# Optimization experiments

Hardware: AMD Instinct MI355X
Metric: run time of the kernel (lower is better)

Reference implementation:

```python
import jax, jax.numpy as jnp
import numpy as np

EMBED = 1024
HEADS = 16
HEAD_DIM = EMBED // HEADS
B, S = 4, 2048


def setup_inputs() -> dict:
    key = jax.random.key(0)
    ks = jax.random.split(key, 13)
    scale = 1.0 / np.sqrt(EMBED)
    inp = {
        "query": jax.random.normal(ks[0], (B, S, EMBED), dtype=jnp.float32),
        "key": jax.random.normal(ks[1], (B, S, EMBED), dtype=jnp.float32),
        "value": jax.random.normal(ks[2], (B, S, EMBED), dtype=jnp.float32),
        "mask": jax.random.randint(ks[3], (B, 1, S, S), 0, 2) > 0,
        "Wq": jax.random.normal(ks[4], (EMBED, EMBED), dtype=jnp.float32) * scale,
        "bq": jnp.zeros((EMBED,), dtype=jnp.float32),
        "Wk": jax.random.normal(ks[5], (EMBED, EMBED), dtype=jnp.float32) * scale,
        "bk": jnp.zeros((EMBED,), dtype=jnp.float32),
        "Wv": jax.random.normal(ks[6], (EMBED, EMBED), dtype=jnp.float32) * scale,
        "bv": jnp.zeros((EMBED,), dtype=jnp.float32),
        "Wo": jax.random.normal(ks[7], (EMBED, EMBED), dtype=jnp.float32) * scale,
        "bo": jnp.zeros((EMBED,), dtype=jnp.float32),
    }
    return inp


def _split_heads(x):
    b, s, _ = x.shape
    return x.reshape(b, s, HEADS, HEAD_DIM).transpose(0, 2, 1, 3)  # [B,H,S,Dh]


def reference(query, key, value, mask, Wq, bq, Wk, bk, Wv, bv, Wo, bo):
    # Linear projections (torch Linear: x @ W.T + b)
    q = _split_heads(query @ Wq.T + bq)
    k = _split_heads(key @ Wk.T + bk)
    v = _split_heads(value @ Wv.T + bv)
    # scaled dot-product attention with full score matrix (as in source)
    scores = jnp.einsum("bhqd,bhkd->bhqk", q, k) / jnp.sqrt(jnp.float32(HEAD_DIM))
    scores = jnp.where(mask, jnp.float32(-1e9), scores)
    attn = jax.nn.softmax(scores, axis=-1)  # dropout p=0 -> identity
    out = jnp.einsum("bhqk,bhkd->bhqd", attn, v)
    out = out.transpose(0, 2, 1, 3).reshape(out.shape[0], -1, EMBED)
    return out @ Wo.T + bo
```

## Files before the change

kernel.cpp:

```cpp
#include <hip/hip_runtime.h>
#include <cstdint>

#define B_  4
#define H_  16
#define S_  2048
#define DH_ 64
#define E_  1024
#define M_  (B_ * S_)

typedef __attribute__((ext_vector_type(8))) __bf16 bf16x8;
typedef __attribute__((ext_vector_type(4))) __bf16 bf16x4;
typedef __attribute__((ext_vector_type(4))) float  f32x4;

__device__ __forceinline__ uint16_t f2bf(float f) {
    union { float f; uint32_t u; } v; v.f = f;
    uint32_t u = v.u;
    uint32_t r = (u + 0x7fffu + ((u >> 16) & 1u)) >> 16;
    return (uint16_t)r;
}
__device__ __forceinline__ uint32_t pack2(float a, float b) {
    return (uint32_t)f2bf(a) | ((uint32_t)f2bf(b) << 16);
}

__device__ __forceinline__ uint32_t cvt_pk_bf16(float lo, float hi) {
    uint32_t r;
    asm("v_cvt_pk_bf16_f32 %0, %1, %2" : "=v"(r) : "v"(lo), "v"(hi));
    return r;
}

__device__ __forceinline__ float exp2_fast(float x) {
#if __has_builtin(__builtin_amdgcn_exp2f)
    return __builtin_amdgcn_exp2f(x);
#else
    float r; asm("v_exp_f32 %0, %1" : "=v"(r) : "v"(x)); return r;
#endif
}

__device__ __forceinline__ void glds16(const void* g, void* lds_base) {
    __builtin_amdgcn_global_load_lds(
        (const __attribute__((address_space(1))) uint32_t*)g,
        (__attribute__((address_space(3))) uint32_t*)lds_base, 16, 0, 0);
}

__global__ void prep_kernel(const float* __restrict__ q, const float* __restrict__ k,
                            const float* __restrict__ v,
                            const float* __restrict__ w0, const float* __restrict__ w1,
                            const float* __restrict__ w2, const float* __restrict__ w3,
                            uint16_t* __restrict__ wbf,
                            uint16_t* __restrict__ qa, uint16_t* __restrict__ ka,
                            uint16_t* __restrict__ va) {
    int bid = blockIdx.x;
    const float* src; uint16_t* dst; int base;
    if (bid < 2048) {
        int i = bid * 256 + threadIdx.x;
        base = i * 8;
        int wsel = base >> 20;
        src = (wsel == 0) ? w0 : (wsel == 1) ? w1 : (wsel == 2) ? w2 : w3;
        dst = wbf + base;
        base &= 1048575;
    } else {
        int r = bid - 2048;
        int sel = r >> 12;
        int i = (r & 4095) * 256 + threadIdx.x;
        base = i * 8;
        src = (sel == 0) ? q : (sel == 1) ? k : v;
        dst = ((sel == 0) ? qa : (sel == 1) ? ka : va) + base;
    }
    float4 a = *(const float4*)(src + base);
    float4 b = *(const float4*)(src + base + 4);
    uint4 o;
    o.x = pack2(a.x, a.y); o.y = pack2(a.z, a.w);
    o.z = pack2(b.x, b.y); o.w = pack2(b.z, b.w);
    *(uint4*)dst = o;
}

__global__ void mask_bits_kernel(const int* __restrict__ mask, uint32_t* __restrict__ bits) {
    int idx = blockIdx.x * 256 + threadIdx.x;
    uint64_t bl = __ballot(mask[idx] != 0);
    if ((threadIdx.x & 63) == 0) {
        int col  = idx & 2047;
        int row  = (idx >> 11) & 2047;
        int b    = idx >> 22;
        int qt8  = row >> 8;
        int rw   = row & 255;
        int w    = rw >> 6, sl = rw & 63;
        int mt   = sl >> 4, quad = (sl >> 2) & 3, r = sl & 3;
        int c0   = col >> 5;
#pragma unroll
        for (int half = 0; half < 2; ++half) {
            int c  = c0 + half;
            int it = c >> 2, js = c & 3;
            size_t i = (((((((size_t)(b * 8 + qt8) * 4 + w) * 4 + js) * 16 + it)
                          * 4 + quad) * 4 + mt) * 4 + r);
            bits[i] = (uint32_t)(half ? (bl >> 32) : bl);
        }
    }
}

__global__ __launch_bounds__(256, 2)
void gemm_bt_kernel(const uint16_t* __restrict__ A0, const uint16_t* __restrict__ A1,
                    const uint16_t* __restrict__ A2,
                    const uint16_t* __restrict__ Bw0,
                    const float* __restrict__ bias0, const float* __restrict__ bias1,
                    const float* __restrict__ bias2,
                    void* __restrict__ out0, void* __restrict__ out1,
                    void* __restrict__ out2,
                    int multi) {
    const int z = blockIdx.z;
    const uint16_t* A  = (z == 0) ? A0 : (z == 1) ? A1 : A2;
    const uint16_t* Bw = Bw0 + (size_t)z * 1048576;
    const float* bias  = (z == 0) ? bias0 : (z == 1) ? bias1 : bias2;
    void* out          = (z == 0) ? out0 : (z == 1) ? out1 : out2;
    const float scale  = (multi && z == 0) ? 0.18033688f : 1.0f;
    const int mode     = multi ? ((z == 2) ? 2 : 1) : 0;

    const int m0 = blockIdx.y * 128;
    const int n0 = blockIdx.x * 128;

    __shared__ __align__(16) uint16_t As[128 * 64];
    __shared__ __align__(16) uint16_t Bs[128 * 64];

    const int t    = threadIdx.x;
    const int w    = t >> 6;
    const int lane = t & 63;
    const int ln   = lane & 15;
    const int quad = lane >> 4;
    const int wr   = w >> 1;
    const int wc   = w & 1;

    f32x4 acc[4][4];
    const f32x4 z4 = {0.f, 0.f, 0.f, 0.f};
#pragma unroll
    for (int i = 0; i < 4; ++i)
#pragma unroll
        for (int j = 0; j < 4; ++j) acc[i][j] = z4;

    const char* Ag = (const char*)(A  + (size_t)m0 * E_);
    const char* Bg = (const char*)(Bw + (size_t)n0 * E_);
    const int rsub = lane >> 3;
    const int colb = ((lane & 7) ^ rsub) * 16;

    for (int kk = 0; kk < E_; kk += 64) {
#pragma unroll
        for (int c = 0; c < 4; ++c) {
            glds16(Ag + (size_t)(c * 32 + w * 8 + rsub) * 2048 + kk * 2 + colb,
                   (char*)As + c * 4096 + w * 1024);
            glds16(Bg + (size_t)(c * 32 + w * 8 + rsub) * 2048 + kk * 2 + colb,
                   (char*)Bs + c * 4096 + w * 1024);
        }
        __syncthreads();

#pragma unroll
        for (int ks = 0; ks < 2; ++ks) {
            bf16x8 af[4], bf[4];
#pragma unroll
            for (int mt = 0; mt < 4; ++mt)
                af[mt] = *(const bf16x8*)&As[(wr * 64 + mt * 16 + ln) * 64 +
                                             (((ks * 4 + quad) ^ (ln & 7)) * 8)];
#pragma unroll
            for (int nt = 0; nt < 4; ++nt)
                bf[nt] = *(const bf16x8*)&Bs[(wc * 64 + nt * 16 + ln) * 64 +
                                             (((ks * 4 + quad) ^ (ln & 7)) * 8)];
#pragma unroll
            for (int mt = 0; mt < 4; ++mt)
#pragma unroll
                for (int nt = 0; nt < 4; ++nt)
                    acc[mt][nt] = __builtin_amdgcn_mfma_f32_16x16x32_bf16(
                        af[mt], bf[nt], acc[mt][nt], 0, 0, 0);
        }
        __syncthreads();
    }

#pragma unroll
    for (int mt = 0; mt < 4; ++mt) {
        const int rowb = m0 + wr * 64 + mt * 16 + quad * 4;
#pragma unroll
        for (int nt = 0; nt < 4; ++nt) {
            const int col = n0 + wc * 64 + nt * 16 + ln;
            const float bsum = bias[col];
            if (mode == 2) {
                int bb = rowb >> 11, s0 = rowb & 2047, hh = col >> 6, d = col & 63;
                float v0 = acc[mt][nt][0] + bsum, v1 = acc[mt][nt][1] + bsum;
                float v2 = acc[mt][nt][2] + bsum, v3 = acc[mt][nt][3] + bsum;
                uint2 o; o.x = pack2(v0, v1); o.y = pack2(v2, v3);
                *(uint2*)((uint16_t*)out + (((size_t)bb * H_ + hh) * DH_ + d) * S_ + s0) = o;
            } else {
#pragma unroll
                for (int r = 0; r < 4; ++r) {
                    float vv = (acc[mt][nt][r] + bsum) * scale;
                    int rr = rowb + r;
                    if (mode == 1) {
                        int bb = rr >> 11, s = rr & 2047, hh = col >> 6, d = col & 63;
                        ((uint16_t*)out)[(((size_t)bb * H_ + hh) * S_ + s) * DH_ + d] = f2bf(vv);
                    } else {
                        ((float*)out)[(size_t)rr * E_ + col] = vv;
                    }
                }
            }
        }
    }
}

__global__ __launch_bounds__(256, 2)
void attn_kernel(const uint16_t* __restrict__ qb, const uint16_t* __restrict__ kb,
                 const uint16_t* __restrict__ vtb, const uint32_t* __restrict__ mbits,
                 uint16_t* __restrict__ attn_out) {
    const int wg   = blockIdx.x;
    const int xcd  = wg & 7;
    const int rest = wg >> 3;
    const int qt8  = rest & 7;
    const int bh   = ((rest >> 3) << 3) | xcd;
    const int b    = bh >> 4, h = bh & 15;

    __shared__ __align__(16) char smem[51200];
    uint16_t* k_lds  = (uint16_t*)smem;
    uint16_t* vt_lds = (uint16_t*)(smem + 16384);
    uint16_t* p_all  = (uint16_t*)(smem + 32768);

    const int t    = threadIdx.x;
    const int w    = t >> 6;
    const int lane = t & 63;
    const int ln   = lane & 15;
    const int quad = lane >> 4;
    const int ln2  = ln << 1;

    const char* qg  = (const char*)(qb  + ((size_t)bh * S_ + qt8 * 256) * DH_);
    const char* kg  = (const char*)(kb  + (size_t)bh * S_ * DH_);
    const char* vtg = (const char*)(vtb + (size_t)bh * DH_ * S_);

    bf16x8 aq[4][2];
#pragma unroll
    for (int mt = 0; mt < 4; ++mt)
#pragma unroll
        for (int ks = 0; ks < 2; ++ks)
            aq[mt][ks] = *(const bf16x8*)(qg + (size_t)(w * 64 + mt * 16 + ln) * 128 +
                                          ks * 64 + quad * 16);

    f32x4 acc_o[4][4];
    const f32x4 z4 = {0.f, 0.f, 0.f, 0.f};
#pragma unroll
    for (int mt = 0; mt < 4; ++mt)
#pragma unroll
        for (int nt = 0; nt < 4; ++nt) acc_o[mt][nt] = z4;
    float lr[4][4];
#pragma unroll
    for (int mt = 0; mt < 4; ++mt)
#pragma unroll
        for (int r = 0; r < 4; ++r) lr[mt][r] = 0.f;

    uint16_t* pw = p_all + w * 2304;
    const uint32_t* mw = mbits + (size_t)(b * 8 + qt8) * 16384 + w * 4096 + quad * 16;

    const int rsub = lane >> 3;
    const int kcol = ((lane & 7) ^ rsub) * 16;

    for (int it = 0; it < 16; ++it) {
        const char* kt = kg + (size_t)it * 16384;
#pragma unroll
        for (int c = 0; c < 4; ++c) {
            const int p    = c * 8 + rsub;
            const int jrow = (p < 16) ? (2 * p) : (2 * p - 31);
            glds16(kt + (size_t)(w * 32 + jrow) * 128 + kcol,
                   (char*)k_lds + w * 4096 + c * 1024);
        }
#pragma unroll
        for (int c = 0; c < 4; ++c) {
            int d0  = w * 16 + c * 4;
            int row = d0 + (lane >> 4);
            int gch = (lane & 15) ^ (row & 15);
            glds16(vtg + (size_t)row * (S_ * 2) + it * 256 + gch * 16,
                   (char*)vt_lds + d0 * 256);
        }
        __syncthreads();

#pragma unroll
        for (int js = 0; js < 4; ++js) {
            uint4 mk4[4];
#pragma unroll
            for (int mt = 0; mt < 4; ++mt)
                mk4[mt] = *(const uint4*)(mw + js * 1024 + it * 64 + mt * 4);
            bf16x8 bv[4];
#pragma unroll
            for (int nt = 0; nt < 4; ++nt)
                bv[nt] = *(const bf16x8*)&vt_lds[(nt * 16 + ln) * 128 +
                                                 (((js * 4 + quad) ^ ln) * 8)];

            f32x4 sc[4][2];
#pragma unroll
            for (int mt = 0; mt < 4; ++mt) { sc[mt][0] = z4; sc[mt][1] = z4; }
#pragma unroll
            for (int ks = 0; ks < 2; ++ks) {
                bf16x8 bk0 = *(const bf16x8*)&k_lds[(js * 32 + ln) * 64 +
                                                    (((ks * 4 + quad) ^ (ln & 7)) * 8)];
                bf16x8 bk1 = *(const bf16x8*)&k_lds[(js * 32 + 16 + ln) * 64 +
                                                    (((ks * 4 + quad) ^ (ln & 7)) * 8)];
#pragma unroll
                for (int mt = 0; mt < 4; ++mt) {
                    sc[mt][0] = __builtin_amdgcn_mfma_f32_16x16x32_bf16(aq[mt][ks], bk0, sc[mt][0], 0, 0, 0);
                    sc[mt][1] = __builtin_amdgcn_mfma_f32_16x16x32_bf16(aq[mt][ks], bk1, sc[mt][1], 0, 0, 0);
                }
            }

#pragma unroll
            for (int mt = 0; mt < 4; ++mt) {
                const uint32_t* mkp = (const uint32_t*)&mk4[mt];
#pragma unroll
                for (int r = 0; r < 4; ++r) {
                    uint32_t sh = mkp[r] >> ln2;
                    float e0 = (sh & 1u) ? 0.f : exp2_fast(sc[mt][0][r]);
                    float e1 = (sh & 2u) ? 0.f : exp2_fast(sc[mt][1][r]);
                    lr[mt][r] += e0 + e1;
                    *(uint32_t*)&pw[(mt * 16 + quad * 4 + r) * 36 + ln2] = cvt_pk_bf16(e0, e1);
                }
            }

#pragma unroll
            for (int mt = 0; mt < 4; ++mt) {
                bf16x4 lo = *(const bf16x4*)&pw[(mt * 16 + ln) * 36 + quad * 8];
                bf16x4 hi = *(const bf16x4*)&pw[(mt * 16 + ln) * 36 + quad * 8 + 4];
                bf16x8 ap = __builtin_shufflevector(lo, hi, 0, 1, 2, 3, 4, 5, 6, 7);
#pragma unroll
                for (int nt = 0; nt < 4; ++nt)
                    acc_o[mt][nt] = __builtin_amdgcn_mfma_f32_16x16x32_bf16(ap, bv[nt], acc_o[mt][nt], 0, 0, 0);
            }
        }
        __syncthreads();
    }

    float invl[4][4];
#pragma unroll
    for (int mt = 0; mt < 4; ++mt)
#pragma unroll
        for (int r = 0; r < 4; ++r) {
            float v = lr[mt][r];
            v += __shfl_xor(v, 1);
            v += __shfl_xor(v, 2);
            v += __shfl_xor(v, 4);
            v += __shfl_xor(v, 8);
            invl[mt][r] = 1.0f / v;
        }

    const size_t orow0 = (size_t)b * S_ + qt8 * 256 + w * 64;
#pragma unroll
    for (int mt = 0; mt < 4; ++mt)
#pragma unroll
        for (int r = 0; r < 4; ++r) {
            const size_t row = orow0 + mt * 16 + quad * 4 + r;
#pragma unroll
            for (int nt = 0; nt < 4; ++nt)
                attn_out[row * E_ + h * 64 + nt * 16 + ln] =
                    f2bf(acc_o[mt][nt][r] * invl[mt][r]);
        }
}

extern "C" void kernel_launch(void* const* d_in, const int* in_sizes, int n_in,
                              void* d_out, int out_size, void* d_ws, size_t ws_size,
                              hipStream_t stream) {
    const float* query = (const float*)d_in[0];
    const float* key_  = (const float*)d_in[1];
    const float* value = (const float*)d_in[2];
    const int*   mask  = (const int*)d_in[3];
    const float* Wq = (const float*)d_in[4];
    const float* bq = (const float*)d_in[5];
    const float* Wk = (const float*)d_in[6];
    const float* bk = (const float*)d_in[7];
    const float* Wv = (const float*)d_in[8];
    const float* bv = (const float*)d_in[9];
    const float* Wo = (const float*)d_in[10];
    const float* bo = (const float*)d_in[11];

    char* ws = (char*)d_ws;
    uint16_t* wbf   = (uint16_t*)ws;
    uint16_t* qa    = (uint16_t*)(ws + (8u   << 20));
    uint16_t* ka    = (uint16_t*)(ws + (24u  << 20));
    uint16_t* va    = (uint16_t*)(ws + (40u  << 20));
    uint16_t* qproj = (uint16_t*)(ws + (56u  << 20));
    uint16_t* kproj = (uint16_t*)(ws + (72u  << 20));
    uint16_t* vtp   = (uint16_t*)(ws + (88u  << 20));
    uint16_t* atto  = (uint16_t*)(ws + (104u << 20));
    uint32_t* mbits = (uint32_t*)(ws + (120u << 20));

    prep_kernel<<<14336, 256, 0, stream>>>(query, key_, value, Wq, Wk, Wv, Wo,
                                           wbf, qa, ka, va);
    mask_bits_kernel<<<65536, 256, 0, stream>>>(mask, mbits);

    gemm_bt_kernel<<<dim3(E_ / 128, M_ / 128, 3), 256, 0, stream>>>(
        qa, ka, va, wbf, bq, bk, bv, qproj, kproj, vtp, 1);

    attn_kernel<<<dim3(512), 256, 0, stream>>>(
        qproj, kproj, vtp, mbits, atto);

    gemm_bt_kernel<<<dim3(E_ / 128, M_ / 128, 1), 256, 0, stream>>>(
        atto, atto, atto, wbf + 3145728, bo, bo, bo, d_out, d_out, d_out, 0);
}
```

Measured before the change: 429.6 us.

## Double-buffer K/V tiles in attention LDS and remap GEMM tile order

The attention kernel now keeps two LDS buffers each for K and V^T. The next tile's global-to-LDS loads are issued before computing on the current tile, which removes the barrier that previously stalled every iteration on a fresh load. To make room, the per-wave P scratch is cut in half, and the softmax/PV step is processed in two halves of two m-tiles each. The projection GEMM also remaps its block index so consecutive workgroups, which land on different XCDs, cover neighbouring m-tiles under the same n-tile, aiming for better L2 reuse of weights. Total LDS grows to about 73 KB per block, which could limit occupancy.

Measured after the change: 419.0 us. 1.03x faster.

```diff
diff --git a/kernel.cpp b/kernel.cpp
--- a/kernel.cpp
+++ b/kernel.cpp
@@ -114,8 +114,9 @@
     const float scale  = (multi && z == 0) ? 0.18033688f : 1.0f;
     const int mode     = multi ? ((z == 2) ? 2 : 1) : 0;
 
-    const int m0 = blockIdx.y * 128;
-    const int n0 = blockIdx.x * 128;
+    const int id  = blockIdx.x + 8 * blockIdx.y;
+    const int m0 = ((id & 7) * 8 + ((id >> 3) & 7)) * 128;
+    const int n0 = (id >> 6) * 128;
 
     __shared__ __align__(16) uint16_t As[128 * 64];
     __shared__ __align__(16) uint16_t Bs[128 * 64];
@@ -212,10 +213,8 @@
     const int bh   = ((rest >> 3) << 3) | xcd;
     const int b    = bh >> 4, h = bh & 15;
 
-    __shared__ __align__(16) char smem[51200];
-    uint16_t* k_lds  = (uint16_t*)smem;
-    uint16_t* vt_lds = (uint16_t*)(smem + 16384);
-    uint16_t* p_all  = (uint16_t*)(smem + 32768);
+    __shared__ __align__(16) char smem[74752];
+    uint16_t* p_all = (uint16_t*)(smem + 65536);
 
     const int t    = threadIdx.x;
     const int w    = t >> 6;
@@ -248,30 +247,41 @@
 #pragma unroll
         for (int r = 0; r < 4; ++r) lr[mt][r] = 0.f;
 
-    uint16_t* pw = p_all + w * 2304;
+    uint16_t* pw = p_all + w * 1152;
     const uint32_t* mw = mbits + (size_t)(b * 8 + qt8) * 16384 + w * 4096 + quad * 16;
 
     const int rsub = lane >> 3;
     const int kcol = ((lane & 7) ^ rsub) * 16;
-
-    for (int it = 0; it < 16; ++it) {
-        const char* kt = kg + (size_t)it * 16384;
+    const int vrow = w * 16 + (lane >> 4);
+
+    auto stage = [&](int tile, int bufsel) {
+        const char* kt = kg + (size_t)tile * 16384;
+        char* kbase = smem + bufsel * 16384 + w * 4096;
 #pragma unroll
         for (int c = 0; c < 4; ++c) {
             const int p    = c * 8 + rsub;
             const int jrow = (p < 16) ? (2 * p) : (2 * p - 31);
-            glds16(kt + (size_t)(w * 32 + jrow) * 128 + kcol,
-                   (char*)k_lds + w * 4096 + c * 1024);
-        }
+            glds16(kt + (size_t)(w * 32 + jrow) * 128 + kcol, kbase + c * 1024);
+        }
+        char* vbase = smem + 32768 + bufsel * 16384;
 #pragma unroll
         for (int c = 0; c < 4; ++c) {
-            int d0  = w * 16 + c * 4;
-            int row = d0 + (lane >> 4);
+            int row = vrow + c * 4;
             int gch = (lane & 15) ^ (row & 15);
-            glds16(vtg + (size_t)row * (S_ * 2) + it * 256 + gch * 16,
-                   (char*)vt_lds + d0 * 256);
-        }
-        __syncthreads();
+            glds16(vtg + (size_t)row * (S_ * 2) + tile * 256 + gch * 16,
+                   vbase + (w * 16 + c * 4) * 256);
+        }
+    };
+
+    stage(0, 0);
+    __syncthreads();
+
+    for (int it = 0; it < 16; ++it) {
+        const int cur = it & 1;
+        if (it < 15) stage(it + 1, cur ^ 1);
+
+        const uint16_t* k_lds  = (const uint16_t*)(smem + cur * 16384);
+        const uint16_t* vt_lds = (const uint16_t*)(smem + 32768 + cur * 16384);
 
 #pragma unroll
         for (int js = 0; js < 4; ++js) {
@@ -302,26 +312,30 @@
             }
 
 #pragma unroll
-            for (int mt = 0; mt < 4; ++mt) {
-                const uint32_t* mkp = (const uint32_t*)&mk4[mt];
-#pragma unroll
-                for (int r = 0; r < 4; ++r) {
-                    uint32_t sh = mkp[r] >> ln2;
-                    float e0 = (sh & 1u) ? 0.f : exp2_fast(sc[mt][0][r]);
-                    float e1 = (sh & 2u) ? 0.f : exp2_fast(sc[mt][1][r]);
-                    lr[mt][r] += e0 + e1;
-                    *(uint32_t*)&pw[(mt * 16 + quad * 4 + r) * 36 + ln2] = cvt_pk_bf16(e0, e1);
+            for (int hf = 0; hf < 2; ++hf) {
+#pragma unroll
+                for (int mh = 0; mh < 2; ++mh) {
+                    const int mt = hf * 2 + mh;
+                    const uint32_t* mkp = (const uint32_t*)&mk4[mt];
+#pragma unroll
+                    for (int r = 0; r < 4; ++r) {
+                        uint32_t sh = mkp[r] >> ln2;
+                        float e0 = (sh & 1u) ? 0.f : exp2_fast(sc[mt][0][r]);
+                        float e1 = (sh & 2u) ? 0.f : exp2_fast(sc[mt][1][r]);
+                        lr[mt][r] += e0 + e1;
+                        *(uint32_t*)&pw[(mh * 16 + quad * 4 + r) * 36 + ln2] = cvt_pk_bf16(e0, e1);
+                    }
                 }
-            }
-
-#pragma unroll
-            for (int mt = 0; mt < 4; ++mt) {
-                bf16x4 lo = *(const bf16x4*)&pw[(mt * 16 + ln) * 36 + quad * 8];
-                bf16x4 hi = *(const bf16x4*)&pw[(mt * 16 + ln) * 36 + quad * 8 + 4];
-                bf16x8 ap = __builtin_shufflevector(lo, hi, 0, 1, 2, 3, 4, 5, 6, 7);
-#pragma unroll
-                for (int nt = 0; nt < 4; ++nt)
-                    acc_o[mt][nt] = __builtin_amdgcn_mfma_f32_16x16x32_bf16(ap, bv[nt], acc_o[mt][nt], 0, 0, 0);
+#pragma unroll
+                for (int mh = 0; mh < 2; ++mh) {
+                    const int mt = hf * 2 + mh;
+                    bf16x4 lo = *(const bf16x4*)&pw[(mh * 16 + ln) * 36 + quad * 8];
+                    bf16x4 hi = *(const bf16x4*)&pw[(mh * 16 + ln) * 36 + quad * 8 + 4];
+                    bf16x8 ap = __builtin_shufflevector(lo, hi, 0, 1, 2, 3, 4, 5, 6, 7);
+#pragma unroll
+                    for (int nt = 0; nt < 4; ++nt)
+                        acc_o[mt][nt] = __builtin_amdgcn_mfma_f32_16x16x32_bf16(ap, bv[nt], acc_o[mt][nt], 0, 0, 0);
+                }
             }
         }
         __syncthreads();
```

## Use 8 waves per attention block, remap GEMM tile order, add MFMA priority hints

Applied to the files above, without the earlier changes.

The attention kernel moves from 4 to 8 waves per 256-row query block. Each wave now owns 32 query rows, and the K/V tile staging is spread across all 8 waves. The mask-bit packing layout is changed to match the new per-wave row split. The GEMM block index is remapped so consecutive blocks share the same N tile across different M tiles, which may improve L2 reuse, and s_setprio hints are wrapped around the MFMA sections. The aim is more latency hiding per CU, at the cost of fewer rows per wave, so each K/V fragment loaded from LDS is reused less.

Measured after the change: 436.0 us. Within noise of the previous version (+1.5%).

```diff
diff --git a/kernel.cpp b/kernel.cpp
--- a/kernel.cpp
+++ b/kernel.cpp
@@ -83,15 +83,15 @@
         int b    = idx >> 22;
         int qt8  = row >> 8;
         int rw   = row & 255;
-        int w    = rw >> 6, sl = rw & 63;
+        int w    = rw >> 5, sl = rw & 31;
         int mt   = sl >> 4, quad = (sl >> 2) & 3, r = sl & 3;
         int c0   = col >> 5;
 #pragma unroll
         for (int half = 0; half < 2; ++half) {
             int c  = c0 + half;
             int it = c >> 2, js = c & 3;
-            size_t i = (((((((size_t)(b * 8 + qt8) * 4 + w) * 4 + js) * 16 + it)
-                          * 4 + quad) * 4 + mt) * 4 + r);
+            size_t i = ((((((size_t)(b * 8 + qt8) * 8 + w) * 4 + js) * 16 + it)
+                         * 4 + quad) * 2 + mt) * 4 + r;
             bits[i] = (uint32_t)(half ? (bl >> 32) : bl);
         }
     }
@@ -114,8 +114,9 @@
     const float scale  = (multi && z == 0) ? 0.18033688f : 1.0f;
     const int mode     = multi ? ((z == 2) ? 2 : 1) : 0;
 
-    const int m0 = blockIdx.y * 128;
-    const int n0 = blockIdx.x * 128;
+    const int id  = blockIdx.x + 8 * blockIdx.y;
+    const int m0 = ((id & 7) * 8 + ((id >> 3) & 7)) * 128;
+    const int n0 = (id >> 6) * 128;
 
     __shared__ __align__(16) uint16_t As[128 * 64];
     __shared__ __align__(16) uint16_t Bs[128 * 64];
@@ -201,7 +202,7 @@
     }
 }
 
-__global__ __launch_bounds__(256, 2)
+__global__ __launch_bounds__(512, 4)
 void attn_kernel(const uint16_t* __restrict__ qb, const uint16_t* __restrict__ kb,
                  const uint16_t* __restrict__ vtb, const uint32_t* __restrict__ mbits,
                  uint16_t* __restrict__ attn_out) {
@@ -213,9 +214,7 @@
     const int b    = bh >> 4, h = bh & 15;
 
     __shared__ __align__(16) char smem[51200];
-    uint16_t* k_lds  = (uint16_t*)smem;
-    uint16_t* vt_lds = (uint16_t*)(smem + 16384);
-    uint16_t* p_all  = (uint16_t*)(smem + 32768);
+    uint16_t* p_all = (uint16_t*)(smem + 32768);
 
     const int t    = threadIdx.x;
     const int w    = t >> 6;
@@ -228,66 +227,75 @@
     const char* kg  = (const char*)(kb  + (size_t)bh * S_ * DH_);
     const char* vtg = (const char*)(vtb + (size_t)bh * DH_ * S_);
 
-    bf16x8 aq[4][2];
-#pragma unroll
-    for (int mt = 0; mt < 4; ++mt)
+    bf16x8 aq[2][2];
+#pragma unroll
+    for (int mt = 0; mt < 2; ++mt)
 #pragma unroll
         for (int ks = 0; ks < 2; ++ks)
-            aq[mt][ks] = *(const bf16x8*)(qg + (size_t)(w * 64 + mt * 16 + ln) * 128 +
+            aq[mt][ks] = *(const bf16x8*)(qg + (size_t)(w * 32 + mt * 16 + ln) * 128 +
                                           ks * 64 + quad * 16);
 
-    f32x4 acc_o[4][4];
+    f32x4 acc_o[2][4];
     const f32x4 z4 = {0.f, 0.f, 0.f, 0.f};
 #pragma unroll
-    for (int mt = 0; mt < 4; ++mt)
+    for (int mt = 0; mt < 2; ++mt)
 #pragma unroll
         for (int nt = 0; nt < 4; ++nt) acc_o[mt][nt] = z4;
-    float lr[4][4];
-#pragma unroll
-    for (int mt = 0; mt < 4; ++mt)
+    float lr[2][4];
+#pragma unroll
+    for (int mt = 0; mt < 2; ++mt)
 #pragma unroll
         for (int r = 0; r < 4; ++r) lr[mt][r] = 0.f;
 
-    uint16_t* pw = p_all + w * 2304;
-    const uint32_t* mw = mbits + (size_t)(b * 8 + qt8) * 16384 + w * 4096 + quad * 16;
+    uint16_t* pw = p_all + w * 1152;
+    const uint32_t* mw = mbits + (size_t)(b * 8 + qt8) * 16384 + w * 2048 + quad * 8;
 
     const int rsub = lane >> 3;
     const int kcol = ((lane & 7) ^ rsub) * 16;
 
+    auto stage = [&](int tile) {
+        const char* kt = kg + (size_t)tile * 16384;
+        char* kbase = smem + w * 2048;
+#pragma unroll
+        for (int c = 0; c < 2; ++c) {
+            const int pr    = w * 16 + c * 8 + rsub;
+            const int strip = pr >> 5, p = pr & 31;
+            const int jrow  = (p < 16) ? (2 * p) : (2 * p - 31);
+            glds16(kt + (size_t)(strip * 32 + jrow) * 128 + kcol, kbase + c * 1024);
+        }
+        char* vbase = smem + 16384 + w * 2048;
+#pragma unroll
+        for (int c = 0; c < 2; ++c) {
+            int row = w * 8 + c * 4 + (lane >> 4);
+            int gch = (lane & 15) ^ (row & 15);
+            glds16(vtg + (size_t)row * (S_ * 2) + tile * 256 + gch * 16,
+                   vbase + c * 1024);
+        }
+    };
+
+    const uint16_t* k_lds  = (const uint16_t*)smem;
+    const uint16_t* vt_lds = (const uint16_t*)(smem + 16384);
+
     for (int it = 0; it < 16; ++it) {
-        const char* kt = kg + (size_t)it * 16384;
-#pragma unroll
-        for (int c = 0; c < 4; ++c) {
-            const int p    = c * 8 + rsub;
-            const int jrow = (p < 16) ? (2 * p) : (2 * p - 31);
-            glds16(kt + (size_t)(w * 32 + jrow) * 128 + kcol,
-                   (char*)k_lds + w * 4096 + c * 1024);
-        }
-#pragma unroll
-        for (int c = 0; c < 4; ++c) {
-            int d0  = w * 16 + c * 4;
-            int row = d0 + (lane >> 4);
-            int gch = (lane & 15) ^ (row & 15);
-            glds16(vtg + (size_t)row * (S_ * 2) + it * 256 + gch * 16,
-                   (char*)vt_lds + d0 * 256);
-        }
+        stage(it);
         __syncthreads();
 
 #pragma unroll
         for (int js = 0; js < 4; ++js) {
-            uint4 mk4[4];
-#pragma unroll
-            for (int mt = 0; mt < 4; ++mt)
-                mk4[mt] = *(const uint4*)(mw + js * 1024 + it * 64 + mt * 4);
+            uint4 mk4[2];
+#pragma unroll
+            for (int mt = 0; mt < 2; ++mt)
+                mk4[mt] = *(const uint4*)(mw + js * 512 + it * 32 + mt * 4);
             bf16x8 bv[4];
 #pragma unroll
             for (int nt = 0; nt < 4; ++nt)
                 bv[nt] = *(const bf16x8*)&vt_lds[(nt * 16 + ln) * 128 +
                                                  (((js * 4 + quad) ^ ln) * 8)];
 
-            f32x4 sc[4][2];
-#pragma unroll
-            for (int mt = 0; mt < 4; ++mt) { sc[mt][0] = z4; sc[mt][1] = z4; }
+            f32x4 sc[2][2];
+#pragma unroll
+            for (int mt = 0; mt < 2; ++mt) { sc[mt][0] = z4; sc[mt][1] = z4; }
+            __builtin_amdgcn_s_setprio(1);
 #pragma unroll
             for (int ks = 0; ks < 2; ++ks) {
                 bf16x8 bk0 = *(const bf16x8*)&k_lds[(js * 32 + ln) * 64 +
@@ -295,14 +303,15 @@
                 bf16x8 bk1 = *(const bf16x8*)&k_lds[(js * 32 + 16 + ln) * 64 +
                                                     (((ks * 4 + quad) ^ (ln & 7)) * 8)];
 #pragma unroll
-                for (int mt = 0; mt < 4; ++mt) {
+                for (int mt = 0; mt < 2; ++mt) {
                     sc[mt][0] = __builtin_amdgcn_mfma_f32_16x16x32_bf16(aq[mt][ks], bk0, sc[mt][0], 0, 0, 0);
                     sc[mt][1] = __builtin_amdgcn_mfma_f32_16x16x32_bf16(aq[mt][ks], bk1, sc[mt][1], 0, 0, 0);
                 }
             }
-
-#pragma unroll
-            for (int mt = 0; mt < 4; ++mt) {
+            __builtin_amdgcn_s_setprio(0);
+
+#pragma unroll
+            for (int mt = 0; mt < 2; ++mt) {
                 const uint32_t* mkp = (const uint32_t*)&mk4[mt];
 #pragma unroll
                 for (int r = 0; r < 4; ++r) {
@@ -314,8 +323,9 @@
                 }
             }
 
-#pragma unroll
-            for (int mt = 0; mt < 4; ++mt) {
+            __builtin_amdgcn_s_setprio(1);
+#pragma unroll
+            for (int mt = 0; mt < 2; ++mt) {
                 bf16x4 lo = *(const bf16x4*)&pw[(mt * 16 + ln) * 36 + quad * 8];
                 bf16x4 hi = *(const bf16x4*)&pw[(mt * 16 + ln) * 36 + quad * 8 + 4];
                 bf16x8 ap = __builtin_shufflevector(lo, hi, 0, 1, 2, 3, 4, 5, 6, 7);
@@ -323,13 +333,14 @@
                 for (int nt = 0; nt < 4; ++nt)
                     acc_o[mt][nt] = __builtin_amdgcn_mfma_f32_16x16x32_bf16(ap, bv[nt], acc_o[mt][nt], 0, 0, 0);
             }
+            __builtin_amdgcn_s_setprio(0);
         }
         __syncthreads();
     }
 
-    float invl[4][4];
-#pragma unroll
-    for (int mt = 0; mt < 4; ++mt)
+    float invl[2][4];
+#pragma unroll
+    for (int mt = 0; mt < 2; ++mt)
 #pragma unroll
         for (int r = 0; r < 4; ++r) {
             float v = lr[mt][r];
@@ -340,9 +351,9 @@
             invl[mt][r] = 1.0f / v;
         }
 
-    const size_t orow0 = (size_t)b * S_ + qt8 * 256 + w * 64;
-#pragma unroll
-    for (int mt = 0; mt < 4; ++mt)
+    const size_t orow0 = (size_t)b * S_ + qt8 * 256 + w * 32;
+#pragma unroll
+    for (int mt = 0; mt < 2; ++mt)
 #pragma unroll
         for (int r = 0; r < 4; ++r) {
             const size_t row = orow0 + mt * 16 + quad * 4 + r;
@@ -387,7 +398,7 @@
     gemm_bt_kernel<<<dim3(E_ / 128, M_ / 128, 3), 256, 0, stream>>>(
         qa, ka, va, wbf, bq, bk, bv, qproj, kproj, vtp, 1);
 
-    attn_kernel<<<dim3(512), 256, 0, stream>>>(
+    attn_kernel<<<dim3(512), 512, 0, stream>>>(
         qproj, kproj, vtp, mbits, atto);
 
     gemm_bt_kernel<<<dim3(E_ / 128, M_ / 128, 1), 256, 0, stream>>>(
```
